# Optimization experiments

Hardware: AMD Instinct MI355X
Metric: run time of the kernel (lower is better)

Reference implementation:

```python
import jax, jax.numpy as jnp
import numpy as np


def setup_inputs() -> dict:
    key = jax.random.key(0)
    ks = jax.random.split(key, 6)
    B, C, H, W = 8, 256, 32, 32
    d = C // 8  # 32
    return {
        "x": jax.random.normal(ks[0], (B, C, H, W), dtype=jnp.float32),
        "Wq": jax.random.normal(ks[1], (d, C), dtype=jnp.float32) * 0.05,
        "bq": jnp.zeros((d,), dtype=jnp.float32),
        "Wk": jax.random.normal(ks[2], (d, C), dtype=jnp.float32) * 0.05,
        "bk": jnp.zeros((d,), dtype=jnp.float32),
        "Wv": jax.random.normal(ks[3], (C, C), dtype=jnp.float32) * 0.05,
        "bv": jnp.zeros((C,), dtype=jnp.float32),
        "Wr": jax.random.normal(ks[4], (d, 2), dtype=jnp.float32) * 0.05,
        "br": jnp.zeros((d,), dtype=jnp.float32),
        "gamma": jnp.array([0.5], dtype=jnp.float32),
    }


def reference(x, Wq, bq, Wk, bk, Wv, bv, Wr, br, gamma):
    B, C, H, W = x.shape
    N = H * W
    d = Wq.shape[0]
    xf = x.reshape(B, C, N)

    # 1x1 convs == per-pixel linear projections
    q = jnp.einsum('dc,bcn->bdn', Wq, xf) + bq[None, :, None]  # (B,d,N)
    k = jnp.einsum('dc,bcn->bdn', Wk, xf) + bk[None, :, None]  # (B,d,N)
    v = jnp.einsum('oc,bcn->bon', Wv, xf) + bv[None, :, None]  # (B,C,N)

    # relative position code: pairwise coord diffs through 1x1 conv (batch-independent)
    gh, gw = jnp.meshgrid(jnp.linspace(0.0, 1.0, H), jnp.linspace(0.0, 1.0, W), indexing='ij')
    coords = jnp.stack([gh.reshape(-1), gw.reshape(-1)])  # (2,N)
    diff = coords[:, :, None] - coords[:, None, :]         # (2,N,N)
    rp_code = jnp.einsum('dt,tij->dij', Wr, diff) + br[:, None, None]  # (d,N,N)

    scale = 1.0 / jnp.sqrt(jnp.asarray(d, dtype=x.dtype))
    score = jnp.einsum('bdi,bdj->bij', q, k) * scale          # (B,N,N)
    rp_score = jnp.einsum('bdi,dij->bij', q, rp_code) * scale  # (B,N,N)
    attn = jax.nn.softmax(score + rp_score, axis=-1)

    # out[b,c,i] = sum_j v[b,c,j] * attn[b,i,j]
    out = jnp.einsum('bcj,bij->bci', v, attn)
    return gamma[0] * out.reshape(B, C, H, W) + x
```

## Files before the change

kernel.cpp:

```cpp
#include <hip/hip_runtime.h>
#include <hip/hip_bf16.h>

#define BATCH 8
#define CH    256
#define NN    1024
#define DD    32

#define QT_OFF 0
#define KT_OFF (BATCH * NN * DD)
#define V_OFF  (2 * BATCH * NN * DD)
#define V2_B   (NN * CH)
#define WF_OFF (V_OFF + BATCH * V2_B)

#define SCALE_Q (0.17677669529663687f * 1.4426950408889634f)
#define INV31 (1.0f / 31.0f)

typedef __attribute__((ext_vector_type(4))) float f32x4;
typedef __attribute__((ext_vector_type(8))) short bf16x8;
typedef __attribute__((ext_vector_type(4))) short bf16x4;

__device__ __forceinline__ unsigned int packbf2(float lo, float hi) {
    __hip_bfloat162 h = __float22bfloat162_rn(make_float2(lo, hi));
    union { __hip_bfloat162 h; unsigned int u; } cv; cv.h = h;
    return cv.u;
}
__device__ __forceinline__ unsigned short f2bf(float x) {
    union { float f; unsigned int u; } v; v.f = x;
    return (unsigned short)((v.u + 0x7FFFu + ((v.u >> 16) & 1u)) >> 16);
}

__global__ __launch_bounds__(256) void wrepack_kernel(
    const float* __restrict__ Wq, const float* __restrict__ Wk,
    const float* __restrict__ Wv, unsigned short* __restrict__ ws)
{
    const int gid = blockIdx.x * 256 + threadIdx.x;
    const int e = gid * 4;
    const int m = e >> 8;
    const int k = e & 255;
    const float* src = (m < 32) ? (Wq + m * CH + k)
                     : (m < 64) ? (Wk + (m - 32) * CH + k)
                                : (Wv + (m - 64) * CH + k);
    const float4 w = *(const float4*)src;
    const int mf = m >> 4, kc = k >> 5;
    const int lf = ((k >> 3) & 3) * 16 + (m & 15);
    const int jj = k & 7;
    uint2 st = { packbf2(w.x, w.y), packbf2(w.z, w.w) };
    *(uint2*)(ws + WF_OFF + ((size_t)(mf * 8 + kc) * 64 + lf) * 8 + jj) = st;
}

__global__ __launch_bounds__(256, 2) void proj_kernel(
    const float* __restrict__ x,
    const float* __restrict__ bq, const float* __restrict__ bk,
    const float* __restrict__ bv, const float* __restrict__ Wr,
    unsigned short* __restrict__ ws)
{
    const int nt   = blockIdx.x;
    const int b    = blockIdx.y;
    const int tid  = threadIdx.x;
    const int wv   = tid >> 6;
    const int lane = tid & 63;
    const int n16  = lane & 15;
    const int q4   = lane >> 4;
    const int n    = nt * 16 + n16;

    f32x4 acc[5];
#pragma unroll
    for (int t = 0; t < 5; t++) acc[t] = (f32x4){0.f, 0.f, 0.f, 0.f};

    const unsigned short* wfl = ws + WF_OFF + (size_t)lane * 8;
    const float* xb = x + (size_t)b * CH * NN + n;

    float  bx[2][8];
    bf16x8 af[2][5];
#pragma unroll
    for (int jj = 0; jj < 8; jj++)
        bx[0][jj] = xb[(size_t)(q4 * 8 + jj) * NN];
#pragma unroll
    for (int t = 0; t < 5; t++)
        af[0][t] = *(const bf16x8*)(wfl + (size_t)((wv * 5 + t) * 8) * 512);

#pragma unroll
    for (int kc = 0; kc < 8; kc++) {
        const int s = kc & 1;
        if (kc < 7) {
            const int kofs = (kc + 1) * 32 + q4 * 8;
#pragma unroll
            for (int jj = 0; jj < 8; jj++)
                bx[s ^ 1][jj] = xb[(size_t)(kofs + jj) * NN];
#pragma unroll
            for (int t = 0; t < 5; t++)
                af[s ^ 1][t] = *(const bf16x8*)(wfl + (size_t)((wv * 5 + t) * 8 + kc + 1) * 512);
        }
        union { unsigned int u[4]; bf16x8 v; } bf;
#pragma unroll
        for (int p = 0; p < 4; p++) bf.u[p] = packbf2(bx[s][2 * p], bx[s][2 * p + 1]);
#pragma unroll
        for (int t = 0; t < 5; t++)
            acc[t] = __builtin_amdgcn_mfma_f32_16x16x32_bf16(af[s][t], bf.v, acc[t], 0, 0, 0);
    }

    const int jj4 = n & 3;
    const int sub = (n >> 4) & 1;
    const int lq  = (n >> 2) & 3;
    const int jt  = n >> 5;
#pragma unroll
    for (int t = 0; t < 5; t++) {
        const int mf = wv * 5 + t;
        const int mb = mf * 16 + q4 * 4;
        if (mb < 32) {
            const float r0 = (acc[t][0] + bq[mb + 0]) * SCALE_Q;
            const float r1 = (acc[t][1] + bq[mb + 1]) * SCALE_Q;
            const float r2 = (acc[t][2] + bq[mb + 2]) * SCALE_Q;
            const float r3 = (acc[t][3] + bq[mb + 3]) * SCALE_Q;
            uint2 st = { packbf2(r0, r1), packbf2(r2, r3) };
            *(uint2*)(ws + QT_OFF + (size_t)(b * NN + n) * DD + mb) = st;
        } else if (mb < 64) {
            const int d = mb - 32;
            const float An = (float)(n >> 5) * INV31;
            const float Bn = (float)(n & 31) * INV31;
            float r[4];
#pragma unroll
            for (int rr = 0; rr < 4; rr++)
                r[rr] = acc[t][rr] + bk[d + rr] - An * Wr[2 * (d + rr)] - Bn * Wr[2 * (d + rr) + 1];
            uint2 st = { packbf2(r[0], r[1]), packbf2(r[2], r[3]) };
            *(uint2*)(ws + KT_OFF + (size_t)(b * NN + n) * DD + d) = st;
        } else {
            const int c = mb - 64;
#pragma unroll
            for (int rr = 0; rr < 4; rr++) {
                const int cc = c + rr;
                const size_t off = V_OFF + (size_t)b * V2_B
                                 + (size_t)jt * 8192 + (size_t)(cc >> 4) * 512
                                 + (size_t)(lq * 16 + (cc & 15)) * 8 + sub * 4 + jj4;
                ws[off] = f2bf(acc[t][rr] + bv[cc]);
            }
        }
    }
}

__global__ __launch_bounds__(256, 4) void attn_kernel(
    const float* __restrict__ x,
    const float* __restrict__ gamma,
    const unsigned short* __restrict__ ws,
    float* __restrict__ out)
{
    const int b    = blockIdx.x;
    const int by   = blockIdx.y;
    const int ig   = by >> 1;
    const int cs   = by & 1;
    const int tid  = threadIdx.x;
    const int jh   = tid >> 7;
    const int cw   = (tid >> 6) & 1;
    const int lane = tid & 63;
    const int n    = lane & 15;
    const int q4   = lane >> 4;
    const int i0   = ig * 16;
    const int cb   = cs * 128 + cw * 64;

    __shared__ float accL[2 * 16 * 64];
    __shared__ float lL[16];

    const unsigned short* qT = ws + QT_OFF + (size_t)b * NN * DD;
    const unsigned short* kT = ws + KT_OFF + (size_t)b * NN * DD + (size_t)jh * 512 * DD;
    const unsigned short* vb = ws + V_OFF + (size_t)b * V2_B
                             + (size_t)jh * 16 * 8192 + (size_t)(cb >> 4) * 512
                             + (size_t)lane * 8;

    const bf16x8 qf = *(const bf16x8*)(qT + (size_t)(i0 + n) * DD + q4 * 8);

    f32x4 acc[4];
#pragma unroll
    for (int t = 0; t < 4; t++) acc[t] = (f32x4){0.f, 0.f, 0.f, 0.f};
    float lsum = 0.f;

    bf16x8 ka0 = *(const bf16x8*)(kT + (size_t)(n) * DD + q4 * 8);
    bf16x8 ka1 = *(const bf16x8*)(kT + (size_t)(16 + n) * DD + q4 * 8);
    bf16x8 va[4];
#pragma unroll
    for (int t = 0; t < 4; t++)
        va[t] = *(const bf16x8*)(vb + t * 512);

#pragma unroll 4
    for (int ch = 0; ch < 16; ch++) {
        const bf16x8 ka0c = ka0, ka1c = ka1;
        bf16x8 vac[4];
#pragma unroll
        for (int t = 0; t < 4; t++) vac[t] = va[t];

        {
            const int j0 = (ch + 1) * 32;
            ka0 = *(const bf16x8*)(kT + (size_t)(j0 + n) * DD + q4 * 8);
            ka1 = *(const bf16x8*)(kT + (size_t)(j0 + 16 + n) * DD + q4 * 8);
#pragma unroll
            for (int t = 0; t < 4; t++)
                va[t] = *(const bf16x8*)(vb + (ch + 1) * 8192 + t * 512);
        }

        const f32x4 z = {0.f, 0.f, 0.f, 0.f};
        f32x4 s0 = __builtin_amdgcn_mfma_f32_16x16x32_bf16(ka0c, qf, z, 0, 0, 0);
        f32x4 s1 = __builtin_amdgcn_mfma_f32_16x16x32_bf16(ka1c, qf, z, 0, 0, 0);

        float p0[4], p1[4];
#pragma unroll
        for (int r = 0; r < 4; r++) {
            p0[r] = exp2f(s0[r]);
            p1[r] = exp2f(s1[r]);
            lsum += p0[r] + p1[r];
        }

        union { unsigned int u[2]; bf16x4 v; } pk0, pk1;
        pk0.u[0] = packbf2(p0[0], p0[1]); pk0.u[1] = packbf2(p0[2], p0[3]);
        pk1.u[0] = packbf2(p1[0], p1[1]); pk1.u[1] = packbf2(p1[2], p1[3]);

#pragma unroll
        for (int t = 0; t < 4; t++) {
            union { bf16x8 w; bf16x4 h[2]; } vs; vs.w = vac[t];
            acc[t] = __builtin_amdgcn_mfma_f32_16x16x16bf16_1k(vs.h[0], pk0.v, acc[t], 0, 0, 0);
            acc[t] = __builtin_amdgcn_mfma_f32_16x16x16bf16_1k(vs.h[1], pk1.v, acc[t], 0, 0, 0);
        }
    }

    lsum += __shfl_xor(lsum, 16, 64);
    lsum += __shfl_xor(lsum, 32, 64);

    if (jh == 1) {
#pragma unroll
        for (int t = 0; t < 4; t++)
#pragma unroll
            for (int r = 0; r < 4; r++)
                accL[(cw * 16 + t * 4 + r) * 64 + lane] = acc[t][r];
        if (cw == 0 && lane < 16) lL[lane] = lsum;
    }
    __syncthreads();

    if (jh == 0) {
        const float rl = gamma[0] / (lsum + lL[n]);
#pragma unroll
        for (int t = 0; t < 4; t++) {
#pragma unroll
            for (int r = 0; r < 4; r++) {
                const int c = cb + t * 16 + q4 * 4 + r;
                const size_t idx = (size_t)(b * CH + c) * NN + i0 + n;
                const float a = acc[t][r] + accL[(cw * 16 + t * 4 + r) * 64 + lane];
                out[idx] = a * rl + x[idx];
            }
        }
    }
}

extern "C" void kernel_launch(void* const* d_in, const int* in_sizes, int n_in,
                              void* d_out, int out_size, void* d_ws, size_t ws_size,
                              hipStream_t stream) {
    (void)in_sizes; (void)n_in; (void)out_size; (void)ws_size;
    const float* x     = (const float*)d_in[0];
    const float* Wq    = (const float*)d_in[1];
    const float* bq    = (const float*)d_in[2];
    const float* Wk    = (const float*)d_in[3];
    const float* bk    = (const float*)d_in[4];
    const float* Wv    = (const float*)d_in[5];
    const float* bv    = (const float*)d_in[6];
    const float* Wr    = (const float*)d_in[7];
    const float* gamma = (const float*)d_in[9];
    float* out = (float*)d_out;
    unsigned short* ws = (unsigned short*)d_ws;

    wrepack_kernel<<<80, 256, 0, stream>>>(Wq, Wk, Wv, ws);
    proj_kernel<<<dim3(64, 8), 256, 0, stream>>>(x, bq, bk, bv, Wr, ws);
    attn_kernel<<<dim3(8, 128), 256, 0, stream>>>(x, gamma, ws, out);
}
```

Measured before the change: 109.6 us.

## Deepen operand prefetch to two stages and split the attention epilogue across both halves

The projection kernel now uses three register buffers and loads x and weight fragments two K-chunks ahead instead of one. The attention kernel likewise prefetches K and V fragments two chunks ahead with a two-slot buffer. In the epilogue, each j-half wave group now finalizes and writes half of the channel tiles, exchanging partial sums through shared memory both ways, so the jh=1 waves no longer sit idle during the reduction. The cost is more live registers, which can lower occupancy. Indexing acc with the runtime value jh may also force the accumulators into scratch memory or select instructions.

```diff
diff --git a/kernel.cpp b/kernel.cpp
--- a/kernel.cpp
+++ b/kernel.cpp
@@ -70,26 +70,31 @@
     const unsigned short* wfl = ws + WF_OFF + (size_t)lane * 8;
     const float* xb = x + (size_t)b * CH * NN + n;
 
-    float  bx[2][8];
-    bf16x8 af[2][5];
-#pragma unroll
-    for (int jj = 0; jj < 8; jj++)
-        bx[0][jj] = xb[(size_t)(q4 * 8 + jj) * NN];
-#pragma unroll
-    for (int t = 0; t < 5; t++)
-        af[0][t] = *(const bf16x8*)(wfl + (size_t)((wv * 5 + t) * 8) * 512);
+    float  bx[3][8];
+    bf16x8 af[3][5];
+#pragma unroll
+    for (int s = 0; s < 2; s++) {
+        const int kofs = s * 32 + q4 * 8;
+#pragma unroll
+        for (int jj = 0; jj < 8; jj++)
+            bx[s][jj] = xb[(size_t)(kofs + jj) * NN];
+#pragma unroll
+        for (int t = 0; t < 5; t++)
+            af[s][t] = *(const bf16x8*)(wfl + (size_t)((wv * 5 + t) * 8 + s) * 512);
+    }
 
 #pragma unroll
     for (int kc = 0; kc < 8; kc++) {
-        const int s = kc & 1;
-        if (kc < 7) {
-            const int kofs = (kc + 1) * 32 + q4 * 8;
+        const int s = kc % 3;
+        if (kc < 6) {
+            const int sp = (kc + 2) % 3;
+            const int kofs = (kc + 2) * 32 + q4 * 8;
 #pragma unroll
             for (int jj = 0; jj < 8; jj++)
-                bx[s ^ 1][jj] = xb[(size_t)(kofs + jj) * NN];
+                bx[sp][jj] = xb[(size_t)(kofs + jj) * NN];
 #pragma unroll
             for (int t = 0; t < 5; t++)
-                af[s ^ 1][t] = *(const bf16x8*)(wfl + (size_t)((wv * 5 + t) * 8 + kc + 1) * 512);
+                af[sp][t] = *(const bf16x8*)(wfl + (size_t)((wv * 5 + t) * 8 + kc + 2) * 512);
         }
         union { unsigned int u[4]; bf16x8 v; } bf;
 #pragma unroll
@@ -157,8 +162,8 @@
     const int i0   = ig * 16;
     const int cb   = cs * 128 + cw * 64;
 
-    __shared__ float accL[2 * 16 * 64];
-    __shared__ float lL[16];
+    __shared__ float accL[2 * 2 * 8 * 64];
+    __shared__ float lL[2][16];
 
     const unsigned short* qT = ws + QT_OFF + (size_t)b * NN * DD;
     const unsigned short* kT = ws + KT_OFF + (size_t)b * NN * DD + (size_t)jh * 512 * DD;
@@ -173,27 +178,33 @@
     for (int t = 0; t < 4; t++) acc[t] = (f32x4){0.f, 0.f, 0.f, 0.f};
     float lsum = 0.f;
 
-    bf16x8 ka0 = *(const bf16x8*)(kT + (size_t)(n) * DD + q4 * 8);
-    bf16x8 ka1 = *(const bf16x8*)(kT + (size_t)(16 + n) * DD + q4 * 8);
-    bf16x8 va[4];
-#pragma unroll
-    for (int t = 0; t < 4; t++)
-        va[t] = *(const bf16x8*)(vb + t * 512);
+    bf16x8 kaS[2][2];
+    bf16x8 vaS[2][4];
+#pragma unroll
+    for (int s = 0; s < 2; s++) {
+        const int j0 = s * 32;
+        kaS[s][0] = *(const bf16x8*)(kT + (size_t)(j0 + n) * DD + q4 * 8);
+        kaS[s][1] = *(const bf16x8*)(kT + (size_t)(j0 + 16 + n) * DD + q4 * 8);
+#pragma unroll
+        for (int t = 0; t < 4; t++)
+            vaS[s][t] = *(const bf16x8*)(vb + s * 8192 + t * 512);
+    }
 
 #pragma unroll 4
     for (int ch = 0; ch < 16; ch++) {
-        const bf16x8 ka0c = ka0, ka1c = ka1;
+        const int st = ch & 1;
+        const bf16x8 ka0c = kaS[st][0], ka1c = kaS[st][1];
         bf16x8 vac[4];
 #pragma unroll
-        for (int t = 0; t < 4; t++) vac[t] = va[t];
+        for (int t = 0; t < 4; t++) vac[t] = vaS[st][t];
 
         {
-            const int j0 = (ch + 1) * 32;
-            ka0 = *(const bf16x8*)(kT + (size_t)(j0 + n) * DD + q4 * 8);
-            ka1 = *(const bf16x8*)(kT + (size_t)(j0 + 16 + n) * DD + q4 * 8);
+            const int j0 = (ch + 2) * 32;
+            kaS[st][0] = *(const bf16x8*)(kT + (size_t)(j0 + n) * DD + q4 * 8);
+            kaS[st][1] = *(const bf16x8*)(kT + (size_t)(j0 + 16 + n) * DD + q4 * 8);
 #pragma unroll
             for (int t = 0; t < 4; t++)
-                va[t] = *(const bf16x8*)(vb + (ch + 1) * 8192 + t * 512);
+                vaS[st][t] = *(const bf16x8*)(vb + (ch + 2) * 8192 + t * 512);
         }
 
         const f32x4 z = {0.f, 0.f, 0.f, 0.f};
@@ -223,25 +234,26 @@
     lsum += __shfl_xor(lsum, 16, 64);
     lsum += __shfl_xor(lsum, 32, 64);
 
-    if (jh == 1) {
-#pragma unroll
-        for (int t = 0; t < 4; t++)
-#pragma unroll
-            for (int r = 0; r < 4; r++)
-                accL[(cw * 16 + t * 4 + r) * 64 + lane] = acc[t][r];
-        if (cw == 0 && lane < 16) lL[lane] = lsum;
-    }
+    const int keep = jh * 2;
+    const int give = 2 - jh * 2;
+#pragma unroll
+    for (int t = 0; t < 2; t++)
+#pragma unroll
+        for (int r = 0; r < 4; r++)
+            accL[(((jh * 2 + cw) * 8) + t * 4 + r) * 64 + lane] = acc[give + t][r];
+    if (cw == 0 && lane < 16) lL[jh][lane] = lsum;
     __syncthreads();
 
-    if (jh == 0) {
-        const float rl = gamma[0] / (lsum + lL[n]);
-#pragma unroll
-        for (int t = 0; t < 4; t++) {
+    {
+        const float rl = gamma[0] / (lsum + lL[1 - jh][n]);
+#pragma unroll
+        for (int t = 0; t < 2; t++) {
 #pragma unroll
             for (int r = 0; r < 4; r++) {
-                const int c = cb + t * 16 + q4 * 4 + r;
+                const int c = cb + (keep + t) * 16 + q4 * 4 + r;
                 const size_t idx = (size_t)(b * CH + c) * NN + i0 + n;
-                const float a = acc[t][r] + accL[(cw * 16 + t * 4 + r) * 64 + lane];
+                const float a = acc[keep + t][r]
+                              + accL[((((1 - jh) * 2 + cw) * 8) + t * 4 + r) * 64 + lane];
                 out[idx] = a * rl + x[idx];
             }
         }
```

Result: slower. 115.8 us (+5.7%).
